# Performance work log

Hardware: AMD Instinct MI355X
Metric: run time of the kernel (lower is better)

## Reference

```python
import jax, jax.numpy as jnp
import numpy as np

IN_N_CH = 32
IN_BS = 1_048_576
IN_SR = 48_000
OUT_SR = 44_100
OUT_BS = -(-IN_BS * OUT_SR // IN_SR)  # ceil -> 963380


def _calc_x_and_indices(in_bs: int, out_bs: int):
    """Faithful port of InplaceLinearResampler.calc_x_and_indices +
    the 4-point neighbor indices from Inplace4pHermiteResampler.set_sample_rates."""
    scaling = (in_bs - 1) / (out_bs - 1) + 1e-12
    xf = np.arange(out_bs, dtype=np.float64) * scaling
    y0 = np.floor(xf).astype(np.int64)
    y1 = np.clip(y0 + 1, 0, in_bs - 1)
    x = np.clip(xf - y0, 0.0, 1.0)
    x[0] = 0.0
    x[-1] = np.round(x[-1])
    y_m1 = np.clip(y0 - 1, 0, in_bs - 1)
    y2 = np.clip(y1 + 1, 0, in_bs - 1)
    return (x.astype(np.float32), y_m1.astype(np.int32), y0.astype(np.int32),
            y1.astype(np.int32), y2.astype(np.int32))


def setup_inputs() -> dict:
    key = jax.random.key(0)
    y = jax.random.normal(key, (IN_N_CH, IN_BS), dtype=jnp.float32)
    x, y_m1_idx, y0_idx, y1_idx, y2_idx = _calc_x_and_indices(IN_BS, OUT_BS)
    return {
        "y": y,
        "x": jnp.asarray(x),
        "y_m1_idx": jnp.asarray(y_m1_idx),
        "y0_idx": jnp.asarray(y0_idx),
        "y1_idx": jnp.asarray(y1_idx),
        "y2_idx": jnp.asarray(y2_idx),
    }


def reference(y, x, y_m1_idx, y0_idx, y1_idx, y2_idx):
    # Gathers: [n_ch, out_bs]
    ym1 = jnp.take(y, y_m1_idx, axis=1)
    y0v = jnp.take(y, y0_idx, axis=1)
    y1v = jnp.take(y, y1_idx, axis=1)
    y2v = jnp.take(y, y2_idx, axis=1)
    # Cubic Hermite coefficients (Niemitalo 4-point, 3rd-order)
    c1 = 0.5 * (y1v - ym1)
    c2 = ym1 - 2.5 * y0v + 2.0 * y1v - 0.5 * y2v
    c3 = 0.5 * (y2v - ym1) + 1.5 * (y0v - y1v)
    # Horner evaluation: ((c3*x + c2)*x + c1)*x + c0, c0 = y0
    return ((c3 * x + c2) * x + c1) * x + y0v
```

## Files before the change

### kernel.cpp

```cpp
#include <hip/hip_runtime.h>
#include <stdint.h>


#define NW    4
#define OPW   256
#define TILE  (NW * OPW)
#define WFL   512
#define CPB   16

typedef float vf4 __attribute__((ext_vector_type(4)));
typedef int   vi4 __attribute__((ext_vector_type(4)));

typedef const __attribute__((address_space(1))) uint32_t* gas_t;
typedef __attribute__((address_space(3))) uint32_t* las_t;

__device__ __forceinline__ void stage2(const float* g, float* l) {
    __builtin_amdgcn_global_load_lds((gas_t)g,         (las_t)l,         16, 0, 0);
    __builtin_amdgcn_global_load_lds((gas_t)(g + 256), (las_t)(l + 256), 16, 0, 0);
}

struct TapIdx { int rm1[4], r0[4], r1[4], r2[4]; };

__device__ __forceinline__ void body(
    int s, const float* __restrict__ gbase, float* op, int out_bs, int in_bs,
    float* cur, float* nxt, const TapIdx& ti, vf4 xv, bool valid, int cpb)
{
    const int sn = (s + 1 < cpb) ? (s + 1) : s;
    stage2(gbase + (size_t)sn * (size_t)in_bs, nxt);
    asm volatile("s_waitcnt vmcnt(2)" ::: "memory");
    __builtin_amdgcn_sched_barrier(0);

    vf4 o;
    #pragma unroll
    for (int k = 0; k < 4; ++k) {
        const float ym1 = cur[ti.rm1[k]];
        const float y0f = cur[ti.r0[k]];
        const float y1f = cur[ti.r1[k]];
        const float y2f = cur[ti.r2[k]];
        const float c1 = 0.5f * (y1f - ym1);
        const float c2 = ym1 - 2.5f * y0f + 2.0f * y1f - 0.5f * y2f;
        const float c3 = 0.5f * (y2f - ym1) + 1.5f * (y0f - y1f);
        const float xw = xv[k];
        o[k] = ((c3 * xw + c2) * xw + c1) * xw + y0f;
    }
    if (valid) *(vf4*)(op + (size_t)s * (size_t)out_bs) = o;
}

__global__ __launch_bounds__(256) void hermite_async_kernel(
    const float* __restrict__ y,
    const float* __restrict__ x,
    const int* __restrict__ y0_idx,
    float* __restrict__ out,
    int out_bs, int in_bs)
{
    __shared__ float sbuf[NW][2][WFL];
    const int t    = threadIdx.x;
    const int w    = t >> 6;
    const int lane = t & 63;
    const int jw   = blockIdx.x * TILE + w * OPW;
    const int j    = jw + 4 * lane;
    const int ch0  = blockIdx.y * CPB;

    int src = (y0_idx[min(jw, out_bs - 1)] - 1) & ~3;
    src = max(src, 0);
    src = min(src, in_bs - WFL);

    const bool valid = (j < out_bs);
    vf4 xv  = {0.f, 0.f, 0.f, 0.f};
    vi4 y0v = {src + 1, src + 1, src + 1, src + 1};
    if (valid) {
        xv  = *(const vf4*)(x + j);
        y0v = *(const vi4*)(y0_idx + j);
    }
    TapIdx ti;
    #pragma unroll
    for (int k = 0; k < 4; ++k) {
        const int y0 = y0v[k];
        ti.rm1[k] = max(y0 - 1, 0) - src;
        ti.r0[k]  = y0 - src;
        ti.r1[k]  = min(y0 + 1, in_bs - 1) - src;
        ti.r2[k]  = min(y0 + 2, in_bs - 1) - src;
    }

    float* lds0 = &sbuf[w][0][0];
    float* lds1 = &sbuf[w][1][0];
    const float* gbase = y + (size_t)ch0 * (size_t)in_bs + src + 4 * lane;
    float*       op    = out + (size_t)ch0 * (size_t)out_bs + j;

    stage2(gbase, lds0);

    for (int s = 0; s < CPB; s += 2) {
        body(s,     gbase, op, out_bs, in_bs, lds0, lds1, ti, xv, valid, CPB);
        body(s + 1, gbase, op, out_bs, in_bs, lds1, lds0, ti, xv, valid, CPB);
    }
}

extern "C" void kernel_launch(void* const* d_in, const int* in_sizes, int n_in,
                              void* d_out, int out_size, void* d_ws, size_t ws_size,
                              hipStream_t stream)
{
    const float* y   = (const float*)d_in[0];
    const float* x   = (const float*)d_in[1];
    const int*   i0  = (const int*)d_in[3];
    float*       out = (float*)d_out;

    const int out_bs = in_sizes[1];
    const int n_ch   = out_size / out_bs;
    const int in_bs  = in_sizes[0] / n_ch;

    dim3 grid((out_bs + TILE - 1) / TILE, n_ch / CPB, 1);
    hermite_async_kernel<<<grid, 256, 0, stream>>>(
        y, x, i0, out, out_bs, in_bs);
}
```

Measured before the change: 54.92 us.

## Deepen LDS prefetch to four buffers, shrink window, add interior fast path

Moves from a double-buffered to a four-buffer LDS pipeline that prefetches three channels ahead, with hand-tuned vmcnt waits. The staged window shrinks from 512 to 320 floats, so only lanes below 16 issue the second async load. An interior specialization reads the four taps as contiguous LDS offsets instead of clamped indices, and output stores become nontemporal. The goal is to hide more global latency and cut redundant traffic, at the cost of more LDS per block and fragile hand-counted wait thresholds.

```diff
diff --git a/kernel.cpp b/kernel.cpp
--- a/kernel.cpp
+++ b/kernel.cpp
@@ -2,11 +2,11 @@
 #include <stdint.h>
 
 
-#define NW    4
-#define OPW   256
-#define TILE  (NW * OPW)
-#define WFL   512
-#define CPB   16
+#define NW   4
+#define OPW  256
+#define TILE (NW * OPW)
+#define WFL  320
+#define CPB  16
 
 typedef float vf4 __attribute__((ext_vector_type(4)));
 typedef int   vi4 __attribute__((ext_vector_type(4)));
@@ -14,46 +14,71 @@
 typedef const __attribute__((address_space(1))) uint32_t* gas_t;
 typedef __attribute__((address_space(3))) uint32_t* las_t;
 
-__device__ __forceinline__ void stage2(const float* g, float* l) {
-    __builtin_amdgcn_global_load_lds((gas_t)g,         (las_t)l,         16, 0, 0);
-    __builtin_amdgcn_global_load_lds((gas_t)(g + 256), (las_t)(l + 256), 16, 0, 0);
+__device__ __forceinline__ void stage_win(const float* g, float* l, int lane) {
+    __builtin_amdgcn_global_load_lds((gas_t)g, (las_t)l, 16, 0, 0);
+    if (lane < 16)
+        __builtin_amdgcn_global_load_lds((gas_t)(g + 256), (las_t)(l + 256), 16, 0, 0);
 }
 
-struct TapIdx { int rm1[4], r0[4], r1[4], r2[4]; };
+template<bool INTERIOR>
+__device__ __forceinline__ void run(
+    const float* __restrict__ gb, float* __restrict__ op, size_t chstride,
+    int out_bs, float* b0, float* b1, float* b2, float* b3, int lane,
+    const int* roff, const int* am1, const int* a1, const int* a2,
+    vf4 xv, bool valid)
+{
+    stage_win(gb + 0 * chstride, b0, lane);
+    stage_win(gb + 1 * chstride, b1, lane);
+    stage_win(gb + 2 * chstride, b2, lane);
 
-__device__ __forceinline__ void body(
-    int s, const float* __restrict__ gbase, float* op, int out_bs, int in_bs,
-    float* cur, float* nxt, const TapIdx& ti, vf4 xv, bool valid, int cpb)
-{
-    const int sn = (s + 1 < cpb) ? (s + 1) : s;
-    stage2(gbase + (size_t)sn * (size_t)in_bs, nxt);
-    asm volatile("s_waitcnt vmcnt(2)" ::: "memory");
-    __builtin_amdgcn_sched_barrier(0);
+#define HBODY(S, CUR, NXT, CNT)                                               \
+  {                                                                           \
+    const int sn = ((S) + 3 < CPB) ? (S) + 3 : CPB - 1;     \
+    stage_win(gb + (size_t)sn * chstride, NXT, lane);                         \
+    asm volatile("s_waitcnt vmcnt(" #CNT ")" ::: "memory");                   \
+    __builtin_amdgcn_sched_barrier(0);                                        \
+    vf4 o;                                                                    \
+    _Pragma("unroll")                                                         \
+    for (int k = 0; k < 4; ++k) {                                             \
+      float ym1, y0f, y1f, y2f;                                               \
+      if (INTERIOR) {                                                         \
+        const float* p = (CUR) + roff[k];                                     \
+        ym1 = p[-1]; y0f = p[0]; y1f = p[1]; y2f = p[2];                      \
+      } else {                                                                \
+        ym1 = (CUR)[am1[k]]; y0f = (CUR)[roff[k]];                            \
+        y1f = (CUR)[a1[k]];  y2f = (CUR)[a2[k]];                              \
+      }                                                                       \
+      const float c1 = 0.5f * (y1f - ym1);                                    \
+      const float c2 = ym1 - 2.5f * y0f + 2.0f * y1f - 0.5f * y2f;            \
+      const float c3 = 0.5f * (y2f - ym1) + 1.5f * (y0f - y1f);               \
+      const float xw = xv[k];                                                 \
+      o[k] = ((c3 * xw + c2) * xw + c1) * xw + y0f;                           \
+    }                                                                         \
+    if (valid)                                                                \
+      __builtin_nontemporal_store(o, (vf4*)(op + (size_t)(S) * (size_t)out_bs)); \
+  }
 
-    vf4 o;
-    #pragma unroll
-    for (int k = 0; k < 4; ++k) {
-        const float ym1 = cur[ti.rm1[k]];
-        const float y0f = cur[ti.r0[k]];
-        const float y1f = cur[ti.r1[k]];
-        const float y2f = cur[ti.r2[k]];
-        const float c1 = 0.5f * (y1f - ym1);
-        const float c2 = ym1 - 2.5f * y0f + 2.0f * y1f - 0.5f * y2f;
-        const float c3 = 0.5f * (y2f - ym1) + 1.5f * (y0f - y1f);
-        const float xw = xv[k];
-        o[k] = ((c3 * xw + c2) * xw + c1) * xw + y0f;
+    HBODY(0, b0, b3, 6)
+    HBODY(1, b1, b0, 7)
+    HBODY(2, b2, b1, 8)
+    HBODY(3, b3, b2, 9)
+    for (int ss = 4; ss < CPB; ss += 4) {
+        HBODY(ss + 0, b0, b3, 9)
+        HBODY(ss + 1, b1, b0, 9)
+        HBODY(ss + 2, b2, b1, 9)
+        HBODY(ss + 3, b3, b2, 9)
     }
-    if (valid) *(vf4*)(op + (size_t)s * (size_t)out_bs) = o;
+#undef HBODY
 }
 
-__global__ __launch_bounds__(256) void hermite_async_kernel(
+__global__ __launch_bounds__(256) void hermite_pipe_kernel(
     const float* __restrict__ y,
     const float* __restrict__ x,
     const int* __restrict__ y0_idx,
     float* __restrict__ out,
     int out_bs, int in_bs)
 {
-    __shared__ float sbuf[NW][2][WFL];
+    __shared__ float sbuf[NW][4][WFL];
     const int t    = threadIdx.x;
     const int w    = t >> 6;
     const int lane = t & 63;
@@ -72,27 +97,31 @@
         xv  = *(const vf4*)(x + j);
         y0v = *(const vi4*)(y0_idx + j);
     }
-    TapIdx ti;
+
+    int roff[4], am1[4], a1[4], a2[4];
     #pragma unroll
     for (int k = 0; k < 4; ++k) {
         const int y0 = y0v[k];
-        ti.rm1[k] = max(y0 - 1, 0) - src;
-        ti.r0[k]  = y0 - src;
-        ti.r1[k]  = min(y0 + 1, in_bs - 1) - src;
-        ti.r2[k]  = min(y0 + 2, in_bs - 1) - src;
+        roff[k] = y0 - src;
+        am1[k]  = max(y0 - 1, 0) - src;
+        a1[k]   = min(y0 + 1, in_bs - 1) - src;
+        a2[k]   = min(y0 + 2, in_bs - 1) - src;
     }
 
-    float* lds0 = &sbuf[w][0][0];
-    float* lds1 = &sbuf[w][1][0];
-    const float* gbase = y + (size_t)ch0 * (size_t)in_bs + src + 4 * lane;
-    float*       op    = out + (size_t)ch0 * (size_t)out_bs + j;
+    const float* gb = y + (size_t)ch0 * (size_t)in_bs + src + 4 * lane;
+    float*       op = out + (size_t)ch0 * (size_t)out_bs + j;
+    float* b0 = &sbuf[w][0][0];
+    float* b1 = &sbuf[w][1][0];
+    float* b2 = &sbuf[w][2][0];
+    float* b3 = &sbuf[w][3][0];
 
-    stage2(gbase, lds0);
-
-    for (int s = 0; s < CPB; s += 2) {
-        body(s,     gbase, op, out_bs, in_bs, lds0, lds1, ti, xv, valid, CPB);
-        body(s + 1, gbase, op, out_bs, in_bs, lds1, lds0, ti, xv, valid, CPB);
-    }
+    const bool interior = (src >= 4) && (src + WFL + 4 <= in_bs);
+    if (interior)
+        run<true >(gb, op, (size_t)in_bs, out_bs, b0, b1, b2, b3, lane,
+                   roff, am1, a1, a2, xv, valid);
+    else
+        run<false>(gb, op, (size_t)in_bs, out_bs, b0, b1, b2, b3, lane,
+                   roff, am1, a1, a2, xv, valid);
 }
 
 extern "C" void kernel_launch(void* const* d_in, const int* in_sizes, int n_in,
@@ -109,6 +138,6 @@
     const int in_bs  = in_sizes[0] / n_ch;
 
     dim3 grid((out_bs + TILE - 1) / TILE, n_ch / CPB, 1);
-    hermite_async_kernel<<<grid, 256, 0, stream>>>(
+    hermite_pipe_kernel<<<grid, 256, 0, stream>>>(
         y, x, i0, out, out_bs, in_bs);
 }
```

New measurement: 48.62 us. 1.13x faster.
